# Performance work log

Measured on AMD Instinct MI355X. Metric: run time of the kernel, lower is better.

Reference implementation:

```python
import jax, jax.numpy as jnp
import numpy as np

N, D, R, NB, E = 50000, 128, 16, 10, 1600000
DECAY_RATE = 0.1
LN_EPS = 1e-5

def setup_inputs() -> dict:
    key = jax.random.key(0)
    ks = jax.random.split(key, 12)
    x = jax.random.normal(ks[0], (N, D), dtype=jnp.float32)
    edge_index = jax.random.randint(ks[1], (2, E), 0, N, dtype=jnp.int64)
    edge_type = jax.random.randint(ks[2], (E,), 0, R, dtype=jnp.int64)
    edge_time = jax.random.uniform(ks[3], (E,), dtype=jnp.float32)
    s = 1.0 / np.sqrt(D)
    basis = jax.random.normal(ks[4], (NB, D, D), dtype=jnp.float32) * s   # RGCN basis matrices
    comp = jax.random.normal(ks[5], (R, NB), dtype=jnp.float32) * (1.0 / np.sqrt(NB))
    root = jax.random.normal(ks[6], (D, D), dtype=jnp.float32) * s        # RGCN self-loop weight
    bias = jnp.zeros((D,), dtype=jnp.float32)
    tp_w = jax.random.normal(ks[7], (D, D), dtype=jnp.float32) * s        # time_proj
    tp_b = jnp.zeros((D,), dtype=jnp.float32)
    gamma = jnp.ones((D,), dtype=jnp.float32)
    beta = jnp.zeros((D,), dtype=jnp.float32)
    return {"x": x, "edge_index": edge_index, "edge_type": edge_type, "edge_time": edge_time,
            "basis": basis, "comp": comp, "root": root, "bias": bias,
            "tp_w": tp_w, "tp_b": tp_b, "gamma": gamma, "beta": beta}

def reference(x, edge_index, edge_type, edge_time, basis, comp, root, bias, tp_w, tp_b, gamma, beta):
    n, d = x.shape
    r = comp.shape[0]
    src, dst = edge_index[0], edge_index[1]
    # ---- RGCNConv (basis decomposition, per-relation mean aggregation) ----
    W = jnp.einsum('rb,bio->rio', comp, basis)                 # [R, D, D]
    msg = x[src]                                               # [E, D] gather
    seg = dst * r + edge_type                                  # combined (node, relation) segment id
    agg = jax.ops.segment_sum(msg, seg, num_segments=n * r)    # [N*R, D]
    cnt = jax.ops.segment_sum(jnp.ones_like(seg, dtype=x.dtype), seg, num_segments=n * r)
    agg = (agg / jnp.maximum(cnt, 1.0)[:, None]).reshape(n, r, d)  # per-relation mean
    x_rgcn = jnp.einsum('nrd,rdo->no', agg, W) + x @ root + bias
    # ---- exponential time decay weights, normalized to sum 1 ----
    td = edge_time.max() - edge_time
    td = td / (td.max() + 1e-8)
    w = jnp.exp(-DECAY_RATE * td)
    w = w / (w.sum() + 1e-8)
    # ---- time-decay aggregation (sum over relations == single scatter-add) ----
    agg_t = jax.ops.segment_sum(msg * w[:, None], dst, num_segments=n)
    deg = jax.ops.segment_sum(jnp.ones_like(dst, dtype=x.dtype), dst, num_segments=n)
    x_time = agg_t / jnp.clip(deg, 1.0)[:, None]
    # ---- combine, relu, (dropout=identity in eval), layernorm ----
    xc = x_rgcn + x_time @ tp_w + tp_b
    h = jax.nn.relu(xc)
    mu = h.mean(-1, keepdims=True)
    var = ((h - mu) ** 2).mean(-1, keepdims=True)
    return (h - mu) * jax.lax.rsqrt(var + LN_EPS) * gamma + beta
```

## Files before the change

### kernel.cpp

```cpp
#include <hip/hip_runtime.h>
#include <hip/hip_bf16.h>
#include <math.h>

#define NN 50000
#define DD 128
#define RR 16
#define NBASIS 10
#define NE 1600000
#define NSEG (NN * RR)
#define NSLICE 12
#define KTOT (NSLICE * DD)
#define DECAY 0.1f

#define NB_COARSE 782
#define NBLK_S 1024
#define EPB 1563
#define NHC (NB_COARSE * NBLK_S)
#define NPART2 (NHC / 1024)
#define FINE 1024
#define CAP 4096

typedef short bf16x8 __attribute__((ext_vector_type(8)));
typedef float f32x4 __attribute__((ext_vector_type(4)));
typedef float f32x2 __attribute__((ext_vector_type(2)));

__device__ __forceinline__ ushort f2b(float f) {
    unsigned u = __float_as_uint(f);
    unsigned r = (u + 0x7FFFu + ((u >> 16) & 1u)) >> 16;
    return (ushort)r;
}
__device__ __forceinline__ unsigned cvt_pk_bf16(float lo, float hi) {
    unsigned r;
    asm("v_cvt_pk_bf16_f32 %0, %1, %2" : "=v"(r) : "v"(lo), "v"(hi));
    return r;
}


#define XB_ITEMS (NN * (DD / 4))
#define PREP_ITEMS (XB_ITEMS + DD * KTOT)
__global__ __launch_bounds__(256) void k_s1(
    const int* __restrict__ edst, const float* __restrict__ t,
    const float* __restrict__ x, const float* __restrict__ basis,
    const float* __restrict__ root, const float* __restrict__ tp_w,
    unsigned* __restrict__ red, unsigned* __restrict__ Hc,
    ushort* __restrict__ xb, ushort* __restrict__ Bt3)
{
    const int bid = blockIdx.x;
    const int tid = threadIdx.x;
    if (bid < NBLK_S) {
        __shared__ unsigned h[NB_COARSE];
        for (int i = tid; i < NB_COARSE; i += 256) h[i] = 0u;
        __syncthreads();
        const int e0 = bid * EPB;
        const int e1 = (e0 + EPB < NE) ? e0 + EPB : NE;
        for (int e = e0 + tid; e < e1; e += 256) {
            int d = __builtin_nontemporal_load(edst + e);
            atomicAdd(&h[d >> 6], 1u);
        }
        __syncthreads();
        for (int i = tid; i < NB_COARSE; i += 256)
            Hc[i * NBLK_S + bid] = h[i];
        return;
    }
    if (bid < NBLK_S + 256) {
        __shared__ float smx[4], smn[4];
        float mx = 0.0f, mn = 1e30f;
        const int stride = 256 * 256;
        for (int i = (bid - NBLK_S) * 256 + tid; i < NE / 4; i += stride) {
            f32x4 v = __builtin_nontemporal_load(((const f32x4*)t) + i);
            mx = fmaxf(mx, fmaxf(fmaxf(v.x, v.y), fmaxf(v.z, v.w)));
            mn = fminf(mn, fminf(fminf(v.x, v.y), fminf(v.z, v.w)));
        }
        for (int o = 32; o >= 1; o >>= 1) {
            mx = fmaxf(mx, __shfl_down(mx, o, 64));
            mn = fminf(mn, __shfl_down(mn, o, 64));
        }
        if ((tid & 63) == 0) { smx[tid >> 6] = mx; smn[tid >> 6] = mn; }
        __syncthreads();
        if (tid == 0) {
            mx = fmaxf(fmaxf(smx[0], smx[1]), fmaxf(smx[2], smx[3]));
            mn = fminf(fminf(smn[0], smn[1]), fminf(smn[2], smn[3]));
            atomicMax(&red[0], __float_as_uint(mx));
            atomicMax(&red[1], ~__float_as_uint(mn));
        }
        return;
    }
    int idx = (bid - NBLK_S - 256) * 256 + tid;
    if (idx < XB_ITEMS) {
        f32x4 v = ((const f32x4*)x)[idx];
        uint2 o;
        o.x = cvt_pk_bf16(v.x, v.y);
        o.y = cvt_pk_bf16(v.z, v.w);
        ((uint2*)xb)[idx] = o;
        return;
    }
    int bidx = idx - XB_ITEMS;
    if (bidx >= DD * KTOT) return;
    int j = bidx / KTOT, k = bidx - j * KTOT;
    int s = k >> 7, d = k & 127;
    float v;
    if (s < NBASIS) {
        v = basis[(s * DD + d) * DD + j];
    } else if (s == NBASIS) {
        v = tp_w[d * DD + j];
    } else {
        v = root[d * DD + j];
    }
    Bt3[bidx] = f2b(v);
}

__global__ __launch_bounds__(1024) void k_scan1(unsigned* __restrict__ Hc,
                                                unsigned* __restrict__ part) {
    __shared__ unsigned sh[1024];
    int tid = threadIdx.x;
    int i = blockIdx.x * 1024 + tid;
    unsigned v = Hc[i];
    sh[tid] = v;
    __syncthreads();
    for (int off = 1; off < 1024; off <<= 1) {
        unsigned t = (tid >= off) ? sh[tid - off] : 0u;
        __syncthreads();
        sh[tid] += t;
        __syncthreads();
    }
    Hc[i] = sh[tid] - v;
    if (tid == 1023) part[blockIdx.x] = sh[1023];
}

__global__ __launch_bounds__(1024) void k_scan2(unsigned* __restrict__ part) {
    __shared__ unsigned sh[1024];
    int tid = threadIdx.x;
    unsigned v = (tid < NPART2) ? part[tid] : 0u;
    sh[tid] = v;
    __syncthreads();
    for (int off = 1; off < 1024; off <<= 1) {
        unsigned t = (tid >= off) ? sh[tid - off] : 0u;
        __syncthreads();
        sh[tid] += t;
        __syncthreads();
    }
    if (tid < NPART2) part[tid] = sh[tid] - v;
}

__global__ __launch_bounds__(1024) void k_scan3(unsigned* __restrict__ Hc,
                                                const unsigned* __restrict__ part) {
    int i = blockIdx.x * 1024 + threadIdx.x;
    Hc[i] += part[i >> 10];
}

__global__ __launch_bounds__(256) void k_s3(
    const int* __restrict__ esrc, const int* __restrict__ edst,
    const int* __restrict__ etype, const float* __restrict__ etime,
    const unsigned* __restrict__ Hc, unsigned* __restrict__ red,
    unsigned long long* __restrict__ tmp)
{
    __shared__ unsigned cur[NB_COARSE];
    __shared__ float ssum[4];
    const int bid = blockIdx.x;
    const int tid = threadIdx.x;
    for (int i = tid; i < NB_COARSE; i += 256)
        cur[i] = Hc[i * NBLK_S + bid];
    const float tmax = __uint_as_float(red[0]);
    const float tmin = __uint_as_float(~red[1]);
    const float rtd = -DECAY / (tmax - tmin + 1e-8f);
    __syncthreads();
    float s = 0.0f;
    const int e0 = bid * EPB;
    const int e1 = (e0 + EPB < NE) ? e0 + EPB : NE;
    for (int e = e0 + tid; e < e1; e += 256) {
        int d    = __builtin_nontemporal_load(edst + e);
        int ty   = __builtin_nontemporal_load(etype + e);
        int sv   = __builtin_nontemporal_load(esrc + e);
        float tv = __builtin_nontemporal_load(etime + e);
        float w = __expf((tmax - tv) * rtd);
        s += w;
        unsigned seg = (unsigned)(d * RR + ty);
        unsigned pos = atomicAdd(&cur[seg >> 10], 1u);
        unsigned lo = (unsigned)(sv & 0xFFFF) | ((unsigned)f2b(w) << 16);
        __builtin_nontemporal_store(
            ((unsigned long long)seg << 32) | lo, tmp + pos);
    }
    for (int o = 32; o >= 1; o >>= 1) s += __shfl_down(s, o, 64);
    if ((tid & 63) == 0) ssum[tid >> 6] = s;
    __syncthreads();
    if (tid == 0)
        atomicAdd(((float*)red) + 2, ssum[0] + ssum[1] + ssum[2] + ssum[3]);
}

__global__ __launch_bounds__(512) void k_s4(
    const unsigned long long* __restrict__ tmp, const unsigned* __restrict__ Hc,
    unsigned* __restrict__ srcw, unsigned* __restrict__ segptr)
{
    __shared__ unsigned long long recs[CAP];
    __shared__ unsigned hist[FINE];
    __shared__ unsigned excl[FINE];
    __shared__ unsigned curf[FINE];
    __shared__ unsigned sh[512];
    const int b = blockIdx.x;
    const int tid = threadIdx.x;
    const unsigned start = Hc[b * NBLK_S];
    const unsigned end   = (b + 1 < NB_COARSE) ? Hc[(b + 1) * NBLK_S] : (unsigned)NE;
    int n = (int)(end - start);
    if (n > CAP) n = CAP;
    for (int i = tid; i < FINE; i += 512) hist[i] = 0u;
    for (int i = tid; i < n; i += 512) recs[i] = tmp[start + i];
    __syncthreads();
    const unsigned base = (unsigned)b << 10;
    for (int i = tid; i < n; i += 512)
        atomicAdd(&hist[(unsigned)(recs[i] >> 32) - base], 1u);
    __syncthreads();
    unsigned a0 = hist[2 * tid], a1 = hist[2 * tid + 1];
    sh[tid] = a0 + a1;
    __syncthreads();
    for (int off = 1; off < 512; off <<= 1) {
        unsigned t = (tid >= off) ? sh[tid - off] : 0u;
        __syncthreads();
        sh[tid] += t;
        __syncthreads();
    }
    unsigned pe = sh[tid] - (a0 + a1);
    excl[2 * tid] = pe;          curf[2 * tid] = pe;
    excl[2 * tid + 1] = pe + a0; curf[2 * tid + 1] = pe + a0;
    __syncthreads();
    for (int i = tid; i < n; i += 512) {
        unsigned long long r = recs[i];
        unsigned p = atomicAdd(&curf[(unsigned)(r >> 32) - base], 1u);
        srcw[start + p] = (unsigned)r;
    }
    for (int i = tid; i < FINE; i += 512)
        segptr[(size_t)b * FINE + i] = start + excl[i];
}

__global__ __launch_bounds__(256) void k_gather(
    const ushort* __restrict__ xb, const unsigned* __restrict__ srcw,
    const unsigned* __restrict__ segptr, const unsigned* __restrict__ red,
    const float* __restrict__ comp,
    ushort* __restrict__ A2)
{
    const int wave = threadIdx.x >> 6, lane = threadIdx.x & 63;
    int dst0 = blockIdx.x * 4 + wave;
    if (dst0 >= NN) return;
    const int dst = __builtin_amdgcn_readfirstlane(dst0);
    const float sumw = ((const float*)red)[2];
    const unsigned s0 = (unsigned)dst * RR;
    const unsigned start = segptr[s0];
    const unsigned endAll = segptr[s0 + RR];
    const unsigned deg = endAll - start;
    unsigned* arow = (unsigned*)(A2 + (size_t)dst * KTOT);
    const unsigned* xbu = (const unsigned*)xb;

    f32x2 cb[NBASIS];
#pragma unroll
    for (int b = 0; b < NBASIS; ++b) cb[b] = (f32x2){0.f, 0.f};
    f32x2 acc = {0.f, 0.f}, xt = {0.f, 0.f};

    int r = 0;
    unsigned scur = start;
    unsigned endr = segptr[s0 + 1];
    unsigned e = start;

#define FLUSH_REL {                                                          \
        float scl = (endr > scur) ? (1.0f / (float)(endr - scur)) : 0.0f;    \
        f32x2 t = acc * scl;                                                 \
        _Pragma("unroll")                                                    \
        for (int b = 0; b < NBASIS; ++b)                                     \
            cb[b] += t * comp[r * NBASIS + b];                               \
        acc = (f32x2){0.f, 0.f}; scur = endr; ++r;                           \
        endr = (r < RR) ? segptr[s0 + r + 1] : 0xFFFFFFFFu; }

#define ACCUM(recq, pvq) {                                                   \
        float wgt = __uint_as_float((recq) & 0xFFFF0000u);                   \
        f32x2 v;                                                             \
        v.x = __uint_as_float((pvq) << 16);                                  \
        v.y = __uint_as_float((pvq) & 0xFFFF0000u);                          \
        acc += v;                                                            \
        xt += v * wgt; }

    while (e < endAll) {
        unsigned idx = e + (unsigned)lane;
        unsigned recv = srcw[(idx < endAll) ? idx : (endAll - 1u)];
        unsigned chunk = endAll - e;
        if (chunk > 64u) chunk = 64u;
        unsigned j = 0;
        for (; j + 8u <= chunk; j += 8u) {
            unsigned rec0 = (unsigned)__builtin_amdgcn_readlane((int)recv, (int)(j + 0));
            unsigned rec1 = (unsigned)__builtin_amdgcn_readlane((int)recv, (int)(j + 1));
            unsigned rec2 = (unsigned)__builtin_amdgcn_readlane((int)recv, (int)(j + 2));
            unsigned rec3 = (unsigned)__builtin_amdgcn_readlane((int)recv, (int)(j + 3));
            unsigned rec4 = (unsigned)__builtin_amdgcn_readlane((int)recv, (int)(j + 4));
            unsigned rec5 = (unsigned)__builtin_amdgcn_readlane((int)recv, (int)(j + 5));
            unsigned rec6 = (unsigned)__builtin_amdgcn_readlane((int)recv, (int)(j + 6));
            unsigned rec7 = (unsigned)__builtin_amdgcn_readlane((int)recv, (int)(j + 7));
            unsigned pv0 = xbu[((rec0 & 0xFFFFu) << 6) + lane];
            unsigned pv1 = xbu[((rec1 & 0xFFFFu) << 6) + lane];
            unsigned pv2 = xbu[((rec2 & 0xFFFFu) << 6) + lane];
            unsigned pv3 = xbu[((rec3 & 0xFFFFu) << 6) + lane];
            unsigned pv4 = xbu[((rec4 & 0xFFFFu) << 6) + lane];
            unsigned pv5 = xbu[((rec5 & 0xFFFFu) << 6) + lane];
            unsigned pv6 = xbu[((rec6 & 0xFFFFu) << 6) + lane];
            unsigned pv7 = xbu[((rec7 & 0xFFFFu) << 6) + lane];
            while (e >= endr) FLUSH_REL; ACCUM(rec0, pv0); ++e;
            while (e >= endr) FLUSH_REL; ACCUM(rec1, pv1); ++e;
            while (e >= endr) FLUSH_REL; ACCUM(rec2, pv2); ++e;
            while (e >= endr) FLUSH_REL; ACCUM(rec3, pv3); ++e;
            while (e >= endr) FLUSH_REL; ACCUM(rec4, pv4); ++e;
            while (e >= endr) FLUSH_REL; ACCUM(rec5, pv5); ++e;
            while (e >= endr) FLUSH_REL; ACCUM(rec6, pv6); ++e;
            while (e >= endr) FLUSH_REL; ACCUM(rec7, pv7); ++e;
        }
        for (; j < chunk; ++j) {
            unsigned rc = (unsigned)__builtin_amdgcn_readlane((int)recv, (int)j);
            unsigned pv = xbu[((rc & 0xFFFFu) << 6) + lane];
            while (e >= endr) FLUSH_REL;
            ACCUM(rc, pv);
            ++e;
        }
    }
    while (r < RR) FLUSH_REL;

#pragma unroll
    for (int b = 0; b < NBASIS; ++b)
        __builtin_nontemporal_store(cvt_pk_bf16(cb[b].x, cb[b].y),
                                    arow + b * 64 + lane);

    float s2 = 1.0f / ((sumw + 1e-8f) * fmaxf((float)deg, 1.0f));
    __builtin_nontemporal_store(cvt_pk_bf16(xt.x * s2, xt.y * s2),
                                arow + NBASIS * 64 + lane);
    __builtin_nontemporal_store(
        ((const unsigned*)(xb + (size_t)dst * DD))[lane],
        arow + (NBASIS + 1) * 64 + lane);
#undef FLUSH_REL
#undef ACCUM
}

__global__ __launch_bounds__(256) void k_fgemm(
    const ushort* __restrict__ A2, const ushort* __restrict__ Bt3,
    const float* __restrict__ bias, const float* __restrict__ tpb,
    const float* __restrict__ gamma, const float* __restrict__ beta,
    float* __restrict__ out)
{
    __shared__ unsigned Bs[2][4096];

    const int tid = threadIdx.x;
    const int w = tid >> 6, lane = tid & 63;
    const int quad = lane >> 4, l16 = lane & 15;
    const int n0 = blockIdx.x * 64;

    f32x4 acc[8];
#pragma unroll
    for (int ct = 0; ct < 8; ++ct) acc[ct] = (f32x4){0.f, 0.f, 0.f, 0.f};

    const ushort* arow = A2 + (size_t)(n0 + w * 16 + l16) * KTOT + quad * 8;
    const int srow = lane >> 3;
    const int sc   = lane & 7;

#define STAGE(buf, itv) {                                                    \
        const int k0_ = (itv) * 64;                                          \
        _Pragma("unroll")                                                    \
        for (int i_ = 0; i_ < 4; ++i_) {                                     \
            const int cid_ = i_ * 4 + w;                                     \
            const int row_ = cid_ * 8 + srow;                                \
            const int ck_  = sc ^ (row_ & 7);                                \
            const ushort* gb_ = Bt3 + (size_t)row_ * KTOT + k0_ + ck_ * 8;   \
            __builtin_amdgcn_global_load_lds(                                \
                (const __attribute__((address_space(1))) unsigned*)gb_,      \
                (__attribute__((address_space(3))) unsigned*)&Bs[buf][cid_ * 256], \
                16, 0, 0);                                                   \
        } }

    STAGE(0, 0);
    bf16x8 afp0 = *(const bf16x8*)(arow);
    bf16x8 afp1 = *(const bf16x8*)(arow + 32);
    __syncthreads();

    const int NIT = KTOT / 64;
    for (int it = 0; it < NIT; ++it) {
        if (it + 1 < NIT) STAGE((it + 1) & 1, it + 1);
        bf16x8 af0 = afp0, af1 = afp1;
        if (it + 1 < NIT) {
            afp0 = *(const bf16x8*)(arow + (it + 1) * 64);
            afp1 = *(const bf16x8*)(arow + (it + 1) * 64 + 32);
        }
        const unsigned* Bp = &Bs[it & 1][0];
#pragma unroll
        for (int ct = 0; ct < 8; ++ct) {
            const int rB = ct * 16 + l16;
            bf16x8 b0 = *(const bf16x8*)&Bp[rB * 32 + ((quad ^ (rB & 7)) << 2)];
            bf16x8 b1 = *(const bf16x8*)&Bp[rB * 32 + (((4 + quad) ^ (rB & 7)) << 2)];
            acc[ct] = __builtin_amdgcn_mfma_f32_16x16x32_bf16(af0, b0, acc[ct], 0, 0, 0);
            acc[ct] = __builtin_amdgcn_mfma_f32_16x16x32_bf16(af1, b1, acc[ct], 0, 0, 0);
        }
        __syncthreads();
    }
#undef STAGE

    float bc[8], gc[8], be[8];
#pragma unroll
    for (int ct = 0; ct < 8; ++ct) {
        int col = ct * 16 + l16;
        bc[ct] = bias[col] + tpb[col];
        gc[ct] = gamma[col];
        be[ct] = beta[col];
    }
    float s[4] = {0, 0, 0, 0}, q[4] = {0, 0, 0, 0};
#pragma unroll
    for (int ct = 0; ct < 8; ++ct)
#pragma unroll
        for (int i = 0; i < 4; ++i) {
            float v = fmaxf(acc[ct][i] + bc[ct], 0.0f);
            acc[ct][i] = v;
            s[i] += v;
            q[i] = fmaf(v, v, q[i]);
        }
#pragma unroll
    for (int off = 1; off < 16; off <<= 1)
#pragma unroll
        for (int i = 0; i < 4; ++i) {
            s[i] += __shfl_xor(s[i], off, 64);
            q[i] += __shfl_xor(q[i], off, 64);
        }
#pragma unroll
    for (int i = 0; i < 4; ++i) {
        const int row = n0 + w * 16 + quad * 4 + i;
        float mu  = s[i] * (1.0f / DD);
        float var = q[i] * (1.0f / DD) - mu * mu;
        float inv = rsqrtf(var + 1e-5f);
        if (row < NN) {
#pragma unroll
            for (int ct = 0; ct < 8; ++ct)
                __builtin_nontemporal_store(
                    (acc[ct][i] - mu) * inv * gc[ct] + be[ct],
                    out + (size_t)row * DD + ct * 16 + l16);
        }
    }
}

extern "C" void kernel_launch(void* const* d_in, const int* in_sizes, int n_in,
                              void* d_out, int out_size, void* d_ws, size_t ws_size,
                              hipStream_t stream)
{
    const float* x     = (const float*)d_in[0];
    const int*   ei    = (const int*)d_in[1];
    const int*   etype = (const int*)d_in[2];
    const float* etime = (const float*)d_in[3];
    const float* basis = (const float*)d_in[4];
    const float* comp  = (const float*)d_in[5];
    const float* root  = (const float*)d_in[6];
    const float* bias  = (const float*)d_in[7];
    const float* tp_w  = (const float*)d_in[8];
    const float* tp_b  = (const float*)d_in[9];
    const float* gamma = (const float*)d_in[10];
    const float* beta  = (const float*)d_in[11];
    float* out = (float*)d_out;

    char* ws = (char*)d_ws;
    size_t off = 0;
    auto alloc = [&](size_t bytes) -> void* {
        void* p = ws + off;
        off = (off + bytes + 255) & ~(size_t)255;
        return p;
    };
    unsigned* red    = (unsigned*)alloc(256);
    unsigned* Hc     = (unsigned*)alloc((size_t)NHC * 4);
    unsigned* part   = (unsigned*)alloc(1024 * 4);
    unsigned* srcw   = (unsigned*)alloc((size_t)NE * 4);
    unsigned long long* tmp = (unsigned long long*)alloc((size_t)NE * 8);
    unsigned* segptr = (unsigned*)alloc((size_t)(NB_COARSE * FINE) * 4);
    ushort*   xb     = (ushort*)alloc((size_t)NN * DD * 2);
    ushort*   Bt3    = (ushort*)alloc((size_t)DD * KTOT * 2);
    ushort*   A2     = (ushort*)alloc((size_t)50048 * KTOT * 2);
    (void)ws_size;

    const int* esrc = ei;
    const int* edst = ei + NE;

    (void)hipMemsetAsync(red, 0, 256, stream);

    const int prep_blocks = (PREP_ITEMS + 255) / 256;
    hipLaunchKernelGGL(k_s1, dim3(NBLK_S + 256 + prep_blocks), dim3(256), 0, stream,
                       edst, etime, x, basis, root, tp_w, red, Hc, xb, Bt3);

    hipLaunchKernelGGL(k_scan1, dim3(NPART2), dim3(1024), 0, stream, Hc, part);
    hipLaunchKernelGGL(k_scan2, dim3(1), dim3(1024), 0, stream, part);
    hipLaunchKernelGGL(k_scan3, dim3(NPART2), dim3(1024), 0, stream, Hc, part);

    hipLaunchKernelGGL(k_s3, dim3(NBLK_S), dim3(256), 0, stream,
                       esrc, edst, etype, etime, Hc, red, tmp);

    hipLaunchKernelGGL(k_s4, dim3(NB_COARSE), dim3(512), 0, stream,
                       tmp, Hc, srcw, segptr);

    hipLaunchKernelGGL(k_gather, dim3((NN + 3) / 4), dim3(256), 0, stream,
                       xb, srcw, segptr, red, comp, A2);

    hipLaunchKernelGGL(k_fgemm, dim3((50048 + 63) / 64), dim3(256), 0, stream,
                       A2, Bt3, bias, tp_b, gamma, beta, out);
}
```

Before: 342.4 us.

## Fold time min/max into histogram pass and fuse scan stages into scatter kernel

The min/max reduction over edge_time now happens inside the per-block histogram loop instead of in 256 separate blocks. The second and third scan kernels are dropped. Each k_s3 block instead redoes the 782-entry scan of per-bucket partials in shared memory and adds it to its own Hc prefix. Block 0 also writes the bucket start offsets for k_s4. This removes two kernel launches and one pass over edge_time, at the cost of redundant small scans in every k_s3 block and scalar time loads in the histogram loop.

```diff
diff --git a/kernel.cpp b/kernel.cpp
--- a/kernel.cpp
+++ b/kernel.cpp
@@ -49,28 +49,22 @@
     const int tid = threadIdx.x;
     if (bid < NBLK_S) {
         __shared__ unsigned h[NB_COARSE];
+        __shared__ float smx[4], smn[4];
         for (int i = tid; i < NB_COARSE; i += 256) h[i] = 0u;
+        float mx = 0.0f, mn = 1e30f;
         __syncthreads();
         const int e0 = bid * EPB;
         const int e1 = (e0 + EPB < NE) ? e0 + EPB : NE;
         for (int e = e0 + tid; e < e1; e += 256) {
-            int d = __builtin_nontemporal_load(edst + e);
+            int d    = __builtin_nontemporal_load(edst + e);
+            float tv = __builtin_nontemporal_load(t + e);
+            mx = fmaxf(mx, tv);
+            mn = fminf(mn, tv);
             atomicAdd(&h[d >> 6], 1u);
         }
         __syncthreads();
         for (int i = tid; i < NB_COARSE; i += 256)
             Hc[i * NBLK_S + bid] = h[i];
-        return;
-    }
-    if (bid < NBLK_S + 256) {
-        __shared__ float smx[4], smn[4];
-        float mx = 0.0f, mn = 1e30f;
-        const int stride = 256 * 256;
-        for (int i = (bid - NBLK_S) * 256 + tid; i < NE / 4; i += stride) {
-            f32x4 v = __builtin_nontemporal_load(((const f32x4*)t) + i);
-            mx = fmaxf(mx, fmaxf(fmaxf(v.x, v.y), fmaxf(v.z, v.w)));
-            mn = fminf(mn, fminf(fminf(v.x, v.y), fminf(v.z, v.w)));
-        }
         for (int o = 32; o >= 1; o >>= 1) {
             mx = fmaxf(mx, __shfl_down(mx, o, 64));
             mn = fminf(mn, __shfl_down(mn, o, 64));
@@ -85,7 +79,7 @@
         }
         return;
     }
-    int idx = (bid - NBLK_S - 256) * 256 + tid;
+    int idx = (bid - NBLK_S) * 256 + tid;
     if (idx < XB_ITEMS) {
         f32x4 v = ((const f32x4*)x)[idx];
         uint2 o;
@@ -127,39 +121,44 @@
     if (tid == 1023) part[blockIdx.x] = sh[1023];
 }
 
-__global__ __launch_bounds__(1024) void k_scan2(unsigned* __restrict__ part) {
-    __shared__ unsigned sh[1024];
-    int tid = threadIdx.x;
-    unsigned v = (tid < NPART2) ? part[tid] : 0u;
-    sh[tid] = v;
-    __syncthreads();
-    for (int off = 1; off < 1024; off <<= 1) {
-        unsigned t = (tid >= off) ? sh[tid - off] : 0u;
-        __syncthreads();
-        sh[tid] += t;
-        __syncthreads();
-    }
-    if (tid < NPART2) part[tid] = sh[tid] - v;
-}
-
-__global__ __launch_bounds__(1024) void k_scan3(unsigned* __restrict__ Hc,
-                                                const unsigned* __restrict__ part) {
-    int i = blockIdx.x * 1024 + threadIdx.x;
-    Hc[i] += part[i >> 10];
-}
-
 __global__ __launch_bounds__(256) void k_s3(
     const int* __restrict__ esrc, const int* __restrict__ edst,
     const int* __restrict__ etype, const float* __restrict__ etime,
-    const unsigned* __restrict__ Hc, unsigned* __restrict__ red,
+    const unsigned* __restrict__ Hc, const unsigned* __restrict__ part,
+    unsigned* __restrict__ red, unsigned* __restrict__ bstart,
     unsigned long long* __restrict__ tmp)
 {
-    __shared__ unsigned cur[NB_COARSE];
+    __shared__ unsigned bp[1024];
+    __shared__ unsigned ts[256];
     __shared__ float ssum[4];
     const int bid = blockIdx.x;
     const int tid = threadIdx.x;
+    for (int i = tid; i < 1024; i += 256)
+        bp[i] = (i < NB_COARSE) ? part[i] : 0u;
+    __syncthreads();
+    unsigned l0 = bp[tid * 4], l1 = bp[tid * 4 + 1],
+             l2 = bp[tid * 4 + 2], l3 = bp[tid * 4 + 3];
+    unsigned lsum = l0 + l1 + l2 + l3;
+    ts[tid] = lsum;
+    __syncthreads();
+    for (int off = 1; off < 256; off <<= 1) {
+        unsigned t = (tid >= off) ? ts[tid - off] : 0u;
+        __syncthreads();
+        ts[tid] += t;
+        __syncthreads();
+    }
+    unsigned base = ts[tid] - lsum;
+    bp[tid * 4]     = base;
+    bp[tid * 4 + 1] = base + l0;
+    bp[tid * 4 + 2] = base + l0 + l1;
+    bp[tid * 4 + 3] = base + l0 + l1 + l2;
+    __syncthreads();
+    if (bid == 0) {
+        for (int i = tid; i < NB_COARSE; i += 256) bstart[i] = bp[i];
+        if (tid == 0) bstart[NB_COARSE] = (unsigned)NE;
+    }
     for (int i = tid; i < NB_COARSE; i += 256)
-        cur[i] = Hc[i * NBLK_S + bid];
+        bp[i] += Hc[i * NBLK_S + bid];
     const float tmax = __uint_as_float(red[0]);
     const float tmin = __uint_as_float(~red[1]);
     const float rtd = -DECAY / (tmax - tmin + 1e-8f);
@@ -175,7 +174,7 @@
         float w = __expf((tmax - tv) * rtd);
         s += w;
         unsigned seg = (unsigned)(d * RR + ty);
-        unsigned pos = atomicAdd(&cur[seg >> 10], 1u);
+        unsigned pos = atomicAdd(&bp[seg >> 10], 1u);
         unsigned lo = (unsigned)(sv & 0xFFFF) | ((unsigned)f2b(w) << 16);
         __builtin_nontemporal_store(
             ((unsigned long long)seg << 32) | lo, tmp + pos);
@@ -188,7 +187,7 @@
 }
 
 __global__ __launch_bounds__(512) void k_s4(
-    const unsigned long long* __restrict__ tmp, const unsigned* __restrict__ Hc,
+    const unsigned long long* __restrict__ tmp, const unsigned* __restrict__ bstart,
     unsigned* __restrict__ srcw, unsigned* __restrict__ segptr)
 {
     __shared__ unsigned long long recs[CAP];
@@ -198,8 +197,8 @@
     __shared__ unsigned sh[512];
     const int b = blockIdx.x;
     const int tid = threadIdx.x;
-    const unsigned start = Hc[b * NBLK_S];
-    const unsigned end   = (b + 1 < NB_COARSE) ? Hc[(b + 1) * NBLK_S] : (unsigned)NE;
+    const unsigned start = bstart[b];
+    const unsigned end   = bstart[b + 1];
     int n = (int)(end - start);
     if (n > CAP) n = CAP;
     for (int i = tid; i < FINE; i += 512) hist[i] = 0u;
@@ -463,6 +462,7 @@
     unsigned* red    = (unsigned*)alloc(256);
     unsigned* Hc     = (unsigned*)alloc((size_t)NHC * 4);
     unsigned* part   = (unsigned*)alloc(1024 * 4);
+    unsigned* bstart = (unsigned*)alloc((NB_COARSE + 1) * 4);
     unsigned* srcw   = (unsigned*)alloc((size_t)NE * 4);
     unsigned long long* tmp = (unsigned long long*)alloc((size_t)NE * 8);
     unsigned* segptr = (unsigned*)alloc((size_t)(NB_COARSE * FINE) * 4);
@@ -477,18 +477,16 @@
     (void)hipMemsetAsync(red, 0, 256, stream);
 
     const int prep_blocks = (PREP_ITEMS + 255) / 256;
-    hipLaunchKernelGGL(k_s1, dim3(NBLK_S + 256 + prep_blocks), dim3(256), 0, stream,
+    hipLaunchKernelGGL(k_s1, dim3(NBLK_S + prep_blocks), dim3(256), 0, stream,
                        edst, etime, x, basis, root, tp_w, red, Hc, xb, Bt3);
 
     hipLaunchKernelGGL(k_scan1, dim3(NPART2), dim3(1024), 0, stream, Hc, part);
-    hipLaunchKernelGGL(k_scan2, dim3(1), dim3(1024), 0, stream, part);
-    hipLaunchKernelGGL(k_scan3, dim3(NPART2), dim3(1024), 0, stream, Hc, part);
 
     hipLaunchKernelGGL(k_s3, dim3(NBLK_S), dim3(256), 0, stream,
-                       esrc, edst, etype, etime, Hc, red, tmp);
+                       esrc, edst, etype, etime, Hc, part, red, bstart, tmp);
 
     hipLaunchKernelGGL(k_s4, dim3(NB_COARSE), dim3(512), 0, stream,
-                       tmp, Hc, srcw, segptr);
+                       tmp, bstart, srcw, segptr);
 
     hipLaunchKernelGGL(k_gather, dim3((NN + 3) / 4), dim3(256), 0, stream,
                        xb, srcw, segptr, red, comp, A2);
```

Measured after the change: 353.1 us. 1.03x slower.
